# Optimization experiments

Measured on AMD Instinct MI355X. Metric: run time of the kernel, lower is better.

The kernel has to match this reference:

```python
import jax, jax.numpy as jnp
import numpy as np

D = 128

def setup_inputs() -> dict:
    key = jax.random.key(0)
    k1, k2, k3, k4, k5, k6, k7 = jax.random.split(key, 7)
    B, L = 2048, 200
    target = jax.random.normal(k1, (B, D), dtype=jnp.float32)
    item_seq = jax.random.normal(k2, (B, L, D), dtype=jnp.float32)
    seq_len = jax.random.randint(k3, (B,), 0, 200, dtype=jnp.int64 if jax.config.jax_enable_x64 else jnp.int32)
    # MLP params: Linear(4D -> 2D), Linear(2D -> 1), PyTorch-style init scale
    s1 = 1.0 / np.sqrt(4 * D)
    s2 = 1.0 / np.sqrt(2 * D)
    W1 = jax.random.uniform(k4, (4 * D, 2 * D), minval=-s1, maxval=s1, dtype=jnp.float32)
    b1 = jax.random.uniform(k5, (2 * D,), minval=-s1, maxval=s1, dtype=jnp.float32)
    W2 = jax.random.uniform(k6, (2 * D, 1), minval=-s2, maxval=s2, dtype=jnp.float32)
    b2 = jax.random.uniform(k7, (1,), minval=-s2, maxval=s2, dtype=jnp.float32)
    return {"target": target, "item_seq": item_seq, "seq_len": seq_len,
            "W1": W1, "b1": b1, "W2": W2, "b2": b2}

def reference(target, item_seq, seq_len, W1, b1, W2, b2):
    B, L, Dd = item_seq.shape
    t = target[:, None, :]                              # B 1 D (broadcast over L)
    tgt = jnp.broadcast_to(t, (B, L, Dd))
    sub = item_seq - tgt
    dot = item_seq * tgt
    mlp_in = jnp.concatenate([tgt, item_seq, sub, dot], axis=-1)   # B L 4D
    h = jax.nn.relu(jnp.einsum('blf,fh->blh', mlp_in, W1) + b1)    # B L 2D
    score = jnp.einsum('blh,ho->blo', h, W2) + b2                  # B L 1
    mask = (jnp.arange(L)[None, :] < seq_len[:, None]).astype(item_seq.dtype)  # B L
    weighted = score * item_seq * mask[:, :, None]                 # B L D
    return jnp.sum(weighted, axis=1)                               # B D
```

## Files before the change

kernel.cpp:

```cpp
#include <hip/hip_runtime.h>
#include <hip/hip_bf16.h>

typedef short short8 __attribute__((ext_vector_type(8)));
typedef float f32x4 __attribute__((ext_vector_type(4)));

#define XSTRIDE 264

static __device__ inline short f2bf(float f) {
    unsigned u = __float_as_uint(f);
    unsigned r = (u + 0x7fffu + ((u >> 16) & 1u)) >> 16;
    return (short)r;
}
static __device__ inline float bf2f(short s) {
    return __uint_as_float(((unsigned)(unsigned short)s) << 16);
}

__global__ void make_wu(const float* __restrict__ W1, float* __restrict__ Wu) {
    int idx = blockIdx.x * 256 + threadIdx.x;
    Wu[idx] = W1[idx] - W1[idx + 256 * 256];
}

__global__ void repack_w(const float* __restrict__ W1, short* __restrict__ Wfrag) {
    int idx = blockIdx.x * 256 + threadIdx.x;
    int j = idx & 7;
    int l = (idx >> 3) & 63;
    int s = (idx >> 9) & 7;
    int t = idx >> 12;
    int k = s * 32 + ((l >> 4) << 3) + j;
    int n = t * 16 + (l & 15);
    float v;
    if (k < 128) v = W1[(128 + k) * 256 + n] + W1[(256 + k) * 256 + n];
    else         v = W1[(384 + (k - 128)) * 256 + n];
    Wfrag[idx] = f2bf(v);
}

__global__ void compute_u(const float* __restrict__ target, const float* __restrict__ Wu,
                          const float* __restrict__ b1, float* __restrict__ U) {
    int b = blockIdx.x;
    int j = threadIdx.x;
    __shared__ float tl[128];
    if (j < 128) tl[j] = target[b * 128 + j];
    __syncthreads();
    float acc = b1[j];
#pragma unroll 8
    for (int d = 0; d < 128; ++d) acc += tl[d] * Wu[d * 256 + j];
    U[b * 256 + j] = acc;
}

__launch_bounds__(256, 2)
__global__ void din_main(const float* __restrict__ target, const float* __restrict__ item_seq,
                         const int* __restrict__ seq_len, const float* __restrict__ W2,
                         const float* __restrict__ b2p, const short* __restrict__ Wfrag,
                         const float* __restrict__ U, float* __restrict__ out) {
    const int b = blockIdx.x;
    const int tid = threadIdx.x;
    const int lane = tid & 63;
    const int wave = tid >> 6;
    const int col = lane & 15;
    const int q = lane >> 4;

    __shared__ __attribute__((aligned(16))) short Xl[16 * XSTRIDE];
    __shared__ float u_s[256];
    __shared__ float w2_s[256];
    __shared__ float scoreP[4][16];
    __shared__ float out_s[128];

    u_s[tid] = U[b * 256 + tid];
    w2_s[tid] = W2[tid];
    const float b2 = b2p[0];
    const int slen = seq_len[b];

    const int r = tid >> 4;
    const int c = (tid & 15) << 3;
    float tgt8[8];
#pragma unroll
    for (int i = 0; i < 8; i++) tgt8[i] = target[b * 128 + c + i];

    short8 bfrag[4][8];
    {
        const short* base = Wfrag + ((size_t)(wave * 32) * 64 + lane) * 8;
#pragma unroll
        for (int i = 0; i < 4; i++)
#pragma unroll
            for (int s = 0; s < 8; s++)
                bfrag[i][s] = *(const short8*)(base + (size_t)((i * 8 + s) * 64) * 8);
    }

    float out_val = 0.f;
    f32x4 acc[4];

    for (int mt = 0; mt < 13; ++mt) {
        const int l0 = mt * 16;
        __syncthreads();

        {
            int lr = l0 + r;
            if (lr > 199) lr = 199;
            const float4* src = (const float4*)(item_seq + ((b * 200 + lr) * 128 + c));
            float4 v0 = src[0], v1 = src[1];
            float v[8] = {v0.x, v0.y, v0.z, v0.w, v1.x, v1.y, v1.z, v1.w};
            short8 p0, p1;
#pragma unroll
            for (int i = 0; i < 8; i++) {
                p0[i] = f2bf(v[i]);
                p1[i] = f2bf(v[i] * tgt8[i]);
            }
            short* xr = Xl + r * XSTRIDE;
            *(short8*)(xr + c) = p0;
            *(short8*)(xr + 128 + c) = p1;
        }
        __syncthreads();

#pragma unroll
        for (int i = 0; i < 4; i++) acc[i] = (f32x4){0.f, 0.f, 0.f, 0.f};

        const short* arow = Xl + col * XSTRIDE + q * 8;
#pragma unroll
        for (int s = 0; s < 8; s++) {
            short8 afrag = *(const short8*)(arow + s * 32);
#pragma unroll
            for (int i = 0; i < 4; i++)
                acc[i] = __builtin_amdgcn_mfma_f32_16x16x32_bf16(afrag, bfrag[i][s], acc[i], 0, 0, 0);
        }

        float sv[4] = {0.f, 0.f, 0.f, 0.f};
#pragma unroll
        for (int i = 0; i < 4; i++) {
            int j = (wave * 4 + i) * 16 + col;
            float uj = u_s[j], wj = w2_s[j];
#pragma unroll
            for (int rg = 0; rg < 4; rg++) {
                float h = acc[i][rg] + uj;
                h = h > 0.f ? h : 0.f;
                sv[rg] += h * wj;
            }
        }
#pragma unroll
        for (int off = 1; off < 16; off <<= 1) {
#pragma unroll
            for (int rg = 0; rg < 4; rg++) sv[rg] += __shfl_xor(sv[rg], off, 64);
        }
        if (col == 0) {
#pragma unroll
            for (int rg = 0; rg < 4; rg++) scoreP[wave][q * 4 + rg] = sv[rg];
        }
        __syncthreads();

        {
            int d = tid & 127;
            int mbase = (tid >> 7) * 8;
#pragma unroll
            for (int mm = 0; mm < 8; mm++) {
                int m = mbase + mm;
                int l = l0 + m;
                float s = scoreP[0][m] + scoreP[1][m] + scoreP[2][m] + scoreP[3][m] + b2;
                s = (l < slen) ? s : 0.f;
                out_val += s * bf2f(Xl[m * XSTRIDE + d]);
            }
        }
    }

    __syncthreads();
    if (tid >= 128) out_s[tid - 128] = out_val;
    __syncthreads();
    if (tid < 128) out[b * 128 + tid] = out_val + out_s[tid];
}

extern "C" void kernel_launch(void* const* d_in, const int* in_sizes, int n_in,
                              void* d_out, int out_size, void* d_ws, size_t ws_size,
                              hipStream_t stream) {
    const float* target   = (const float*)d_in[0];
    const float* item_seq = (const float*)d_in[1];
    const int*   seq_len  = (const int*)d_in[2];
    const float* W1       = (const float*)d_in[3];
    const float* b1       = (const float*)d_in[4];
    const float* W2       = (const float*)d_in[5];
    const float* b2       = (const float*)d_in[6];
    float* out = (float*)d_out;

    char* ws = (char*)d_ws;
    float* Wu    = (float*)ws;
    short* Wfrag = (short*)(ws + 131072);
    float* U     = (float*)(ws + 262144);

    make_wu<<<128, 256, 0, stream>>>(W1, Wu);
    repack_w<<<256, 256, 0, stream>>>(W1, Wfrag);
    compute_u<<<2048, 256, 0, stream>>>(target, Wu, b1, U);
    din_main<<<2048, 256, 0, stream>>>(target, item_seq, seq_len, W2, b2, Wfrag, U, out);
}
```

Baseline: 363.7 us.

## Fuse U computation into main kernel, skip masked tiles, prefetch next tile

Moves the per-batch target projection (U = target·Wu + b1) into the main kernel, which removes one kernel launch and the U round trip through global memory. The sequence loop now runs only over tiles that cover seq_len instead of all 13. The next tile's item_seq loads are issued before the current tile's MFMA work so load latency overlaps with compute. Each block now does its own 128x256 matvec reading Wu from global/L2, which adds per-block work before the main loop.

```diff
diff --git a/kernel.cpp b/kernel.cpp
--- a/kernel.cpp
+++ b/kernel.cpp
@@ -34,24 +34,12 @@
     Wfrag[idx] = f2bf(v);
 }
 
-__global__ void compute_u(const float* __restrict__ target, const float* __restrict__ Wu,
-                          const float* __restrict__ b1, float* __restrict__ U) {
-    int b = blockIdx.x;
-    int j = threadIdx.x;
-    __shared__ float tl[128];
-    if (j < 128) tl[j] = target[b * 128 + j];
-    __syncthreads();
-    float acc = b1[j];
-#pragma unroll 8
-    for (int d = 0; d < 128; ++d) acc += tl[d] * Wu[d * 256 + j];
-    U[b * 256 + j] = acc;
-}
-
 __launch_bounds__(256, 2)
 __global__ void din_main(const float* __restrict__ target, const float* __restrict__ item_seq,
                          const int* __restrict__ seq_len, const float* __restrict__ W2,
                          const float* __restrict__ b2p, const short* __restrict__ Wfrag,
-                         const float* __restrict__ U, float* __restrict__ out) {
+                         const float* __restrict__ Wu, const float* __restrict__ b1,
+                         float* __restrict__ out) {
     const int b = blockIdx.x;
     const int tid = threadIdx.x;
     const int lane = tid & 63;
@@ -60,21 +48,44 @@
     const int q = lane >> 4;
 
     __shared__ __attribute__((aligned(16))) short Xl[16 * XSTRIDE];
+    __shared__ __attribute__((aligned(16))) float tshared[128];
     __shared__ float u_s[256];
     __shared__ float w2_s[256];
     __shared__ float scoreP[4][16];
     __shared__ float out_s[128];
 
-    u_s[tid] = U[b * 256 + tid];
-    w2_s[tid] = W2[tid];
+    const int slen = seq_len[b];
+    const int ntiles = (slen + 15) >> 4;
     const float b2 = b2p[0];
-    const int slen = seq_len[b];
 
     const int r = tid >> 4;
     const int c = (tid & 15) << 3;
+
+    float4 v0, v1;
+    if (ntiles > 0) {
+        int lr = r;
+        const float4* src = (const float4*)(item_seq + (((size_t)b * 200 + lr) * 128 + c));
+        v0 = src[0]; v1 = src[1];
+    }
+
+    if (tid < 128) tshared[tid] = target[b * 128 + tid];
+    w2_s[tid] = W2[tid];
+    __syncthreads();
+
+    {
+        float uacc = b1[tid];
+#pragma unroll 8
+        for (int d = 0; d < 128; ++d) uacc += tshared[d] * Wu[d * 256 + tid];
+        u_s[tid] = uacc;
+    }
+
     float tgt8[8];
-#pragma unroll
-    for (int i = 0; i < 8; i++) tgt8[i] = target[b * 128 + c + i];
+    {
+        const float4* t4 = (const float4*)(tshared + c);
+        float4 ta = t4[0], tb = t4[1];
+        tgt8[0] = ta.x; tgt8[1] = ta.y; tgt8[2] = ta.z; tgt8[3] = ta.w;
+        tgt8[4] = tb.x; tgt8[5] = tb.y; tgt8[6] = tb.z; tgt8[7] = tb.w;
+    }
 
     short8 bfrag[4][8];
     {
@@ -89,15 +100,11 @@
     float out_val = 0.f;
     f32x4 acc[4];
 
-    for (int mt = 0; mt < 13; ++mt) {
+    for (int mt = 0; mt < ntiles; ++mt) {
         const int l0 = mt * 16;
         __syncthreads();
 
         {
-            int lr = l0 + r;
-            if (lr > 199) lr = 199;
-            const float4* src = (const float4*)(item_seq + ((b * 200 + lr) * 128 + c));
-            float4 v0 = src[0], v1 = src[1];
             float v[8] = {v0.x, v0.y, v0.z, v0.w, v1.x, v1.y, v1.z, v1.w};
             short8 p0, p1;
 #pragma unroll
@@ -110,6 +117,13 @@
             *(short8*)(xr + 128 + c) = p1;
         }
         __syncthreads();
+
+        if (mt + 1 < ntiles) {
+            int lr = l0 + 16 + r;
+            if (lr > 199) lr = 199;
+            const float4* src = (const float4*)(item_seq + (((size_t)b * 200 + lr) * 128 + c));
+            v0 = src[0]; v1 = src[1];
+        }
 
 #pragma unroll
         for (int i = 0; i < 4; i++) acc[i] = (f32x4){0.f, 0.f, 0.f, 0.f};
@@ -181,10 +195,8 @@
     char* ws = (char*)d_ws;
     float* Wu    = (float*)ws;
     short* Wfrag = (short*)(ws + 131072);
-    float* U     = (float*)(ws + 262144);
 
     make_wu<<<128, 256, 0, stream>>>(W1, Wu);
     repack_w<<<256, 256, 0, stream>>>(W1, Wfrag);
-    compute_u<<<2048, 256, 0, stream>>>(target, Wu, b1, U);
-    din_main<<<2048, 256, 0, stream>>>(target, item_seq, seq_len, W2, b2, Wfrag, U, out);
-}
+    din_main<<<2048, 256, 0, stream>>>(target, item_seq, seq_len, W2, b2, Wfrag, Wu, b1, out);
+}
```

After: 334.8 us. 1.09x faster.
